# Optimization experiments

Hardware: AMD Instinct MI355X
Metric: run time of the kernel (lower is better)

The kernel has to match this reference:

```python
import jax, jax.numpy as jnp
import numpy as np

N = 100000   # nodes
DEG = 32     # in-degree per node
E = N * DEG  # 3.2M edges
D = 24       # node feature dim
NK = 2       # number of anisotropic kernels (tile(...,2) in source forces 2)
H = 64       # MLP hidden/out channels


def setup_inputs() -> dict:
    key = jax.random.key(0)
    k1, k2, k3, k4 = jax.random.split(key, 4)
    x = jax.random.normal(k1, (N, D), dtype=jnp.float32)
    src = jax.random.randint(k2, (E,), 0, N)
    tgt = jnp.repeat(jnp.arange(N), DEG)  # every node has DEG in-edges -> no 0/0
    edge_index = jnp.stack([src, tgt]).astype(jnp.int64)
    kvals = jax.random.normal(k3, (NK, E), dtype=jnp.float32)
    # Linear(2*D -> H, bias=False), xavier-like scale
    W = jax.random.normal(k4, (H, NK * D), dtype=jnp.float32) * (1.0 / (NK * D))
    return {"x": x, "edge_index": edge_index, "kvals": kvals, "W": W}


def reference(x, edge_index, kvals, W):
    src, tgt = edge_index[0], edge_index[1]
    xs = x[src]  # [E, D] gathered source features
    # per-kernel sparse aggregation: out_k[i] = sum_{e: tgt[e]==i} kvals[k,e] * x[src[e]]
    out = jnp.concatenate(
        [jax.ops.segment_sum(kvals[k][:, None] * xs, tgt, num_segments=N)
         for k in range(NK)], axis=1)  # [N, NK*D]
    # adj_norm: subtract tiled neighbor mean
    deg = jax.ops.segment_sum(jnp.ones((E,), x.dtype), tgt, num_segments=N)  # [N]
    sum_x = jax.ops.segment_sum(xs, tgt, num_segments=N)  # [N, D]
    norm_x = sum_x / deg[:, None]
    out = out - jnp.tile(norm_x, (1, NK)) + jnp.tile(x, (1, NK))
    # MLP: single bias-free linear, no activation
    return out @ W.T  # [N, H]
```

## Files before the change

kernel.cpp:

```cpp
#include <hip/hip_runtime.h>


#define NN   100000
#define DEG  32
#define EE   (NN * DEG)
#define DD   24
#define HH   64
#define NPB  32
#define TPB  256
#define NPW  8
#define PST  56

typedef __attribute__((ext_vector_type(8)))  short short8;
typedef __attribute__((ext_vector_type(16))) float float16;
typedef __attribute__((ext_vector_type(4)))  float f32x4;
typedef __attribute__((ext_vector_type(4)))  int   i32x4;
typedef __attribute__((ext_vector_type(4)))  unsigned short u16x4;

__device__ __forceinline__ unsigned short f2bf(float f) {
    union { float f; unsigned u; } v; v.f = f;
    unsigned r = v.u + 0x7fffu + ((v.u >> 16) & 1u);
    return (unsigned short)(r >> 16);
}

__device__ __forceinline__ float bf2f(unsigned u) {
    union { unsigned i; float f; } v; v.i = u << 16; return v.f;
}

__device__ __forceinline__ unsigned pk(unsigned a, unsigned b) {
    return __builtin_amdgcn_perm(b, a, 0x05040100u);
}

__device__ __forceinline__ short8 mk8(unsigned u0, unsigned u1, unsigned u2, unsigned u3) {
    union { unsigned u[4]; short8 s; } p;
    p.u[0] = u0; p.u[1] = u1; p.u[2] = u2; p.u[3] = u3;
    return p.s;
}

__global__ void xcvt(const float* __restrict__ x, unsigned short* __restrict__ xb, int n4) {
    int i = blockIdx.x * blockDim.x + threadIdx.x;
    if (i < n4) {
        f32x4 v = __builtin_nontemporal_load(((const f32x4*)x) + i);
        u16x4 o;
        o.x = f2bf(v.x); o.y = f2bf(v.y); o.z = f2bf(v.z); o.w = f2bf(v.w);
        __builtin_nontemporal_store(o, ((u16x4*)xb) + i);
    }
}

__global__ __launch_bounds__(TPB, 4) void gnn(
    const unsigned short* __restrict__ xb,
    const int*            __restrict__ ei,
    const float*          __restrict__ kv,
    const float*          __restrict__ W,
    float*                __restrict__ out)
{
    __shared__ int            ei_s[NPB * DEG];
    __shared__ unsigned short kv_s[2 * NPB * DEG];
    __shared__ unsigned short pre_s[NPB * PST];

    const int t    = threadIdx.x;
    const int lane = t & 63;
    const int w    = t >> 6;
    const int m    = lane & 31;
    const int kh   = lane >> 5;
    const int kh8  = kh * 8;
    const int base = blockIdx.x * NPB;
    const int dclamp = (m < DD) ? m : (DD - 1);
    const int m2     = dclamp * 2;
    const char* xbc  = (const char*)xb;

    {
        const size_t eb = (size_t)base * DEG;
        i32x4 ev = __builtin_nontemporal_load(((const i32x4*)(ei + eb)) + t);
        ev.x *= 48; ev.y *= 48; ev.z *= 48; ev.w *= 48;
        ((i32x4*)ei_s)[t] = ev;
        const f32x4 c0 = __builtin_nontemporal_load(((const f32x4*)(kv + eb)) + t);
        const f32x4 c1 = __builtin_nontemporal_load(((const f32x4*)(kv + EE + eb)) + t);
        u16x4 u0, u1;
        u0.x = f2bf(c0.x); u0.y = f2bf(c0.y); u0.z = f2bf(c0.z); u0.w = f2bf(c0.w);
        u1.x = f2bf(c1.x); u1.y = f2bf(c1.y); u1.z = f2bf(c1.z); u1.w = f2bf(c1.w);
        ((u16x4*)kv_s)[t] = u0;
        ((u16x4*)(kv_s + NPB * DEG))[t] = u1;
    }
    __syncthreads();

    const unsigned short* kvrow = kv_s + (m & 1) * (NPB * DEG);

    unsigned g[3][16];
    unsigned xv[3];

    #define LOAD_NODE(nl, sl) do {                                             \
        const int el_ = (nl) * DEG + kh8;                                      \
        const i32x4 s0_ = *(const i32x4*)(ei_s + el_);                         \
        const i32x4 s1_ = *(const i32x4*)(ei_s + el_ + 4);                     \
        const i32x4 s2_ = *(const i32x4*)(ei_s + el_ + 16);                    \
        const i32x4 s3_ = *(const i32x4*)(ei_s + el_ + 20);                    \
        g[sl][0]  = *(const unsigned short*)(xbc + (unsigned)(s0_.x + m2));    \
        g[sl][1]  = *(const unsigned short*)(xbc + (unsigned)(s0_.y + m2));    \
        g[sl][2]  = *(const unsigned short*)(xbc + (unsigned)(s0_.z + m2));    \
        g[sl][3]  = *(const unsigned short*)(xbc + (unsigned)(s0_.w + m2));    \
        g[sl][4]  = *(const unsigned short*)(xbc + (unsigned)(s1_.x + m2));    \
        g[sl][5]  = *(const unsigned short*)(xbc + (unsigned)(s1_.y + m2));    \
        g[sl][6]  = *(const unsigned short*)(xbc + (unsigned)(s1_.z + m2));    \
        g[sl][7]  = *(const unsigned short*)(xbc + (unsigned)(s1_.w + m2));    \
        g[sl][8]  = *(const unsigned short*)(xbc + (unsigned)(s2_.x + m2));    \
        g[sl][9]  = *(const unsigned short*)(xbc + (unsigned)(s2_.y + m2));    \
        g[sl][10] = *(const unsigned short*)(xbc + (unsigned)(s2_.z + m2));    \
        g[sl][11] = *(const unsigned short*)(xbc + (unsigned)(s2_.w + m2));    \
        g[sl][12] = *(const unsigned short*)(xbc + (unsigned)(s3_.x + m2));    \
        g[sl][13] = *(const unsigned short*)(xbc + (unsigned)(s3_.y + m2));    \
        g[sl][14] = *(const unsigned short*)(xbc + (unsigned)(s3_.z + m2));    \
        g[sl][15] = *(const unsigned short*)(xbc + (unsigned)(s3_.w + m2));    \
        xv[sl] = xb[(base + (nl)) * DD + dclamp];                              \
    } while (0)

    LOAD_NODE(w * NPW + 0, 0);
    LOAD_NODE(w * NPW + 1, 1);

    #pragma unroll
    for (int i = 0; i < NPW; ++i) {
        const int cur = i % 3;
        const int nl  = w * NPW + i;
        if (i < NPW - 2) LOAD_NODE(nl + 2, (i + 2) % 3);

        const int el = nl * DEG + kh8;
        const short8 raw0 = *(const short8*)(kvrow + el);
        const short8 raw1 = *(const short8*)(kvrow + el + 16);
        const unsigned fill = (m == 2) ? 0x3F803F80u : 0u;
        const short8 af0 = (m < 2) ? raw0 : mk8(fill, fill, fill, fill);
        const short8 af1 = (m < 2) ? raw1 : mk8(fill, fill, fill, fill);

        const short8 bf0 = mk8(pk(g[cur][0],  g[cur][1]),  pk(g[cur][2],  g[cur][3]),
                               pk(g[cur][4],  g[cur][5]),  pk(g[cur][6],  g[cur][7]));
        const short8 bf1 = mk8(pk(g[cur][8],  g[cur][9]),  pk(g[cur][10], g[cur][11]),
                               pk(g[cur][12], g[cur][13]), pk(g[cur][14], g[cur][15]));

        float16 acc;
        #pragma unroll
        for (int r = 0; r < 16; ++r) acc[r] = 0.f;
        acc = __builtin_amdgcn_mfma_f32_32x32x16_bf16(af0, bf0, acc, 0, 0, 0);
        acc = __builtin_amdgcn_mfma_f32_32x32x16_bf16(af1, bf1, acc, 0, 0, 0);

        if (kh == 0 && m < DD) {
            const float sm = acc[2] * (1.f / 32.f);
            const float pv = bf2f(xv[cur]) - sm;
            pre_s[nl * PST + m]      = f2bf(acc[0] + pv);
            pre_s[nl * PST + 24 + m] = f2bf(acc[1] + pv);
        }
    }
    #undef LOAD_NODE
    __syncthreads();

    if (w < 2) {
        const int h = w * 32 + m;

        float16 acc;
        #pragma unroll
        for (int r = 0; r < 16; ++r) acc[r] = 0.f;

        #pragma unroll
        for (int kc = 0; kc < 3; ++kc) {
            const int c0 = kc * 16 + kh8;
            const short8 af = *(const short8*)(pre_s + m * PST + c0);
            const float* wr = W + h * 48 + c0;
            const f32x4 wA = ((const f32x4*)wr)[0];
            const f32x4 wB = ((const f32x4*)wr)[1];
            const short8 bf = mk8(pk(f2bf(wA.x), f2bf(wA.y)), pk(f2bf(wA.z), f2bf(wA.w)),
                                  pk(f2bf(wB.x), f2bf(wB.y)), pk(f2bf(wB.z), f2bf(wB.w)));
            acc = __builtin_amdgcn_mfma_f32_32x32x16_bf16(af, bf, acc, 0, 0, 0);
        }

        #pragma unroll
        for (int r = 0; r < 16; ++r) {
            const int row = (r & 3) + 8 * (r >> 2) + 4 * kh;
            __builtin_nontemporal_store(acc[r], &out[(size_t)(base + row) * HH + h]);
        }
    }
}

extern "C" void kernel_launch(void* const* d_in, const int* in_sizes, int n_in,
                              void* d_out, int out_size, void* d_ws, size_t ws_size,
                              hipStream_t stream) {
    const float* x  = (const float*)d_in[0];
    const int*   ei = (const int*)d_in[1];
    const float* kv = (const float*)d_in[2];
    const float* W  = (const float*)d_in[3];
    float* out = (float*)d_out;

    unsigned short* xb = (unsigned short*)d_ws;
    const int n4 = NN * DD / 4;
    xcvt<<<(n4 + 255) / 256, 256, 0, stream>>>(x, xb, n4);

    const int grid = NN / NPB;
    gnn<<<grid, TPB, 0, stream>>>(xb, ei, kv, W, out);
}
```

Measured before the change: 131.3 us.

## Gather neighbor rows as 16-byte vectors into swizzled LDS before MFMA

The bf16 copy of x is padded to 32-element (64-byte) rows, so each lane can fetch a 16-byte chunk of a neighbor row instead of issuing many 2-byte scalar gathers. Each wave gathers two nodes' neighbor rows into a per-wave shared-memory staging buffer with an XOR swizzle, then reads the bf16 elements back out to build the MFMA operands, double-buffering the gathers in registers. The aim is fewer, wider global loads. In exchange it uses extra LDS (16 KB per block), which may reduce occupancy, and adds LDS round trips. The padded tail of each row is never written, so those bytes hold whatever was already in the workspace and are read as garbage columns; this looks harmless only because the clamped column index (up to 23) never reaches them.

```diff
diff --git a/kernel.cpp b/kernel.cpp
--- a/kernel.cpp
+++ b/kernel.cpp
@@ -10,6 +10,7 @@
 #define TPB  256
 #define NPW  8
 #define PST  56
+#define XRU  32
 
 typedef __attribute__((ext_vector_type(8)))  short short8;
 typedef __attribute__((ext_vector_type(16))) float float16;
@@ -37,13 +38,15 @@
     return p.s;
 }
 
-__global__ void xcvt(const float* __restrict__ x, unsigned short* __restrict__ xb, int n4) {
-    int i = blockIdx.x * blockDim.x + threadIdx.x;
-    if (i < n4) {
-        f32x4 v = __builtin_nontemporal_load(((const f32x4*)x) + i);
+__global__ void xcvt(const float* __restrict__ x, unsigned short* __restrict__ xb, int n6) {
+    int c = blockIdx.x * blockDim.x + threadIdx.x;
+    if (c < n6) {
+        int row = c / 6;
+        int pos = c - row * 6;
+        f32x4 v = __builtin_nontemporal_load(((const f32x4*)x) + c);
         u16x4 o;
         o.x = f2bf(v.x); o.y = f2bf(v.y); o.z = f2bf(v.z); o.w = f2bf(v.w);
-        __builtin_nontemporal_store(o, ((u16x4*)xb) + i);
+        ((u16x4*)xb)[row * 8 + pos] = o;
     }
 }
 
@@ -57,6 +60,7 @@
     __shared__ int            ei_s[NPB * DEG];
     __shared__ unsigned short kv_s[2 * NPB * DEG];
     __shared__ unsigned short pre_s[NPB * PST];
+    __shared__ unsigned short xs_s[4][64 * XRU];
 
     const int t    = threadIdx.x;
     const int lane = t & 63;
@@ -69,10 +73,16 @@
     const int m2     = dclamp * 2;
     const char* xbc  = (const char*)xb;
 
+    const int er   = lane >> 2;
+    const int q16  = (lane & 3) * 16;
+    char* xsb = (char*)&xs_s[w][0];
+    const unsigned wswz = (unsigned)((lane & 32) << 1);
+    const unsigned fswz = (unsigned)(kh << 6);
+
     {
         const size_t eb = (size_t)base * DEG;
         i32x4 ev = __builtin_nontemporal_load(((const i32x4*)(ei + eb)) + t);
-        ev.x *= 48; ev.y *= 48; ev.z *= 48; ev.w *= 48;
+        ev.x <<= 6; ev.y <<= 6; ev.z <<= 6; ev.w <<= 6;
         ((i32x4*)ei_s)[t] = ev;
         const f32x4 c0 = __builtin_nontemporal_load(((const f32x4*)(kv + eb)) + t);
         const f32x4 c1 = __builtin_nontemporal_load(((const f32x4*)(kv + EE + eb)) + t);
@@ -86,69 +96,76 @@
 
     const unsigned short* kvrow = kv_s + (m & 1) * (NPB * DEG);
 
-    unsigned g[3][16];
-    unsigned xv[3];
-
-    #define LOAD_NODE(nl, sl) do {                                             \
-        const int el_ = (nl) * DEG + kh8;                                      \
-        const i32x4 s0_ = *(const i32x4*)(ei_s + el_);                         \
-        const i32x4 s1_ = *(const i32x4*)(ei_s + el_ + 4);                     \
-        const i32x4 s2_ = *(const i32x4*)(ei_s + el_ + 16);                    \
-        const i32x4 s3_ = *(const i32x4*)(ei_s + el_ + 20);                    \
-        g[sl][0]  = *(const unsigned short*)(xbc + (unsigned)(s0_.x + m2));    \
-        g[sl][1]  = *(const unsigned short*)(xbc + (unsigned)(s0_.y + m2));    \
-        g[sl][2]  = *(const unsigned short*)(xbc + (unsigned)(s0_.z + m2));    \
-        g[sl][3]  = *(const unsigned short*)(xbc + (unsigned)(s0_.w + m2));    \
-        g[sl][4]  = *(const unsigned short*)(xbc + (unsigned)(s1_.x + m2));    \
-        g[sl][5]  = *(const unsigned short*)(xbc + (unsigned)(s1_.y + m2));    \
-        g[sl][6]  = *(const unsigned short*)(xbc + (unsigned)(s1_.z + m2));    \
-        g[sl][7]  = *(const unsigned short*)(xbc + (unsigned)(s1_.w + m2));    \
-        g[sl][8]  = *(const unsigned short*)(xbc + (unsigned)(s2_.x + m2));    \
-        g[sl][9]  = *(const unsigned short*)(xbc + (unsigned)(s2_.y + m2));    \
-        g[sl][10] = *(const unsigned short*)(xbc + (unsigned)(s2_.z + m2));    \
-        g[sl][11] = *(const unsigned short*)(xbc + (unsigned)(s2_.w + m2));    \
-        g[sl][12] = *(const unsigned short*)(xbc + (unsigned)(s3_.x + m2));    \
-        g[sl][13] = *(const unsigned short*)(xbc + (unsigned)(s3_.y + m2));    \
-        g[sl][14] = *(const unsigned short*)(xbc + (unsigned)(s3_.z + m2));    \
-        g[sl][15] = *(const unsigned short*)(xbc + (unsigned)(s3_.w + m2));    \
-        xv[sl] = xb[(base + (nl)) * DD + dclamp];                              \
+    i32x4 G[2][4];
+    unsigned short xvv[2][2];
+
+    #define GATHER_GANG(gg, sl) do {                                           \
+        const int eb_ = (w * NPW + 2 * (gg)) * DEG;                            \
+        const int o0_ = ei_s[eb_ +  0 + er];                                   \
+        const int o1_ = ei_s[eb_ + 16 + er];                                   \
+        const int o2_ = ei_s[eb_ + 32 + er];                                   \
+        const int o3_ = ei_s[eb_ + 48 + er];                                   \
+        G[sl][0] = *(const i32x4*)(xbc + (unsigned)(o0_ + q16));               \
+        G[sl][1] = *(const i32x4*)(xbc + (unsigned)(o1_ + q16));               \
+        G[sl][2] = *(const i32x4*)(xbc + (unsigned)(o2_ + q16));               \
+        G[sl][3] = *(const i32x4*)(xbc + (unsigned)(o3_ + q16));               \
+        xvv[sl][0] = xb[(base + w * NPW + 2 * (gg)) * XRU + dclamp];           \
+        xvv[sl][1] = xb[(base + w * NPW + 2 * (gg) + 1) * XRU + dclamp];       \
     } while (0)
 
-    LOAD_NODE(w * NPW + 0, 0);
-    LOAD_NODE(w * NPW + 1, 1);
+    #define WRITE_GANG(sl) do {                                                \
+        *(i32x4*)(xsb + (((0 * 1024) + er * 64 + q16) ^ wswz)) = G[sl][0];     \
+        *(i32x4*)(xsb + (((1 * 1024) + er * 64 + q16) ^ wswz)) = G[sl][1];     \
+        *(i32x4*)(xsb + (((2 * 1024) + er * 64 + q16) ^ wswz)) = G[sl][2];     \
+        *(i32x4*)(xsb + (((3 * 1024) + er * 64 + q16) ^ wswz)) = G[sl][3];     \
+    } while (0)
+
+    #define COMPUTE_NODE(nn, gg, sl) do {                                      \
+        const int nl_ = w * NPW + 2 * (gg) + (nn);                             \
+        const char* fb_ = xsb + (nn) * 2048 + (kh << 9);                       \
+        unsigned ga_[8], gb_[8];                                               \
+        _Pragma("unroll")                                                      \
+        for (int j = 0; j < 8; ++j)                                            \
+            ga_[j] = *(const unsigned short*)(fb_ + (((j << 6) + m2) ^ fswz)); \
+        _Pragma("unroll")                                                      \
+        for (int j = 0; j < 8; ++j)                                            \
+            gb_[j] = *(const unsigned short*)(fb_ + 1024 + (((j << 6) + m2) ^ fswz)); \
+        const int el_ = nl_ * DEG + kh8;                                       \
+        const short8 raw0_ = *(const short8*)(kvrow + el_);                    \
+        const short8 raw1_ = *(const short8*)(kvrow + el_ + 16);               \
+        const unsigned fill_ = (m == 2) ? 0x3F803F80u : 0u;                    \
+        const short8 af0_ = (m < 2) ? raw0_ : mk8(fill_, fill_, fill_, fill_); \
+        const short8 af1_ = (m < 2) ? raw1_ : mk8(fill_, fill_, fill_, fill_); \
+        const short8 bf0_ = mk8(pk(ga_[0], ga_[1]), pk(ga_[2], ga_[3]),        \
+                                pk(ga_[4], ga_[5]), pk(ga_[6], ga_[7]));       \
+        const short8 bf1_ = mk8(pk(gb_[0], gb_[1]), pk(gb_[2], gb_[3]),        \
+                                pk(gb_[4], gb_[5]), pk(gb_[6], gb_[7]));       \
+        float16 acc_;                                                          \
+        _Pragma("unroll")                                                      \
+        for (int r = 0; r < 16; ++r) acc_[r] = 0.f;                            \
+        acc_ = __builtin_amdgcn_mfma_f32_32x32x16_bf16(af0_, bf0_, acc_, 0, 0, 0); \
+        acc_ = __builtin_amdgcn_mfma_f32_32x32x16_bf16(af1_, bf1_, acc_, 0, 0, 0); \
+        if (kh == 0 && m < DD) {                                               \
+            const float sm_ = acc_[2] * (1.f / 32.f);                          \
+            const float pv_ = bf2f(xvv[sl][nn]) - sm_;                         \
+            pre_s[nl_ * PST + m]      = f2bf(acc_[0] + pv_);                   \
+            pre_s[nl_ * PST + 24 + m] = f2bf(acc_[1] + pv_);                   \
+        }                                                                      \
+    } while (0)
+
+    GATHER_GANG(0, 0);
 
     #pragma unroll
-    for (int i = 0; i < NPW; ++i) {
-        const int cur = i % 3;
-        const int nl  = w * NPW + i;
-        if (i < NPW - 2) LOAD_NODE(nl + 2, (i + 2) % 3);
-
-        const int el = nl * DEG + kh8;
-        const short8 raw0 = *(const short8*)(kvrow + el);
-        const short8 raw1 = *(const short8*)(kvrow + el + 16);
-        const unsigned fill = (m == 2) ? 0x3F803F80u : 0u;
-        const short8 af0 = (m < 2) ? raw0 : mk8(fill, fill, fill, fill);
-        const short8 af1 = (m < 2) ? raw1 : mk8(fill, fill, fill, fill);
-
-        const short8 bf0 = mk8(pk(g[cur][0],  g[cur][1]),  pk(g[cur][2],  g[cur][3]),
-                               pk(g[cur][4],  g[cur][5]),  pk(g[cur][6],  g[cur][7]));
-        const short8 bf1 = mk8(pk(g[cur][8],  g[cur][9]),  pk(g[cur][10], g[cur][11]),
-                               pk(g[cur][12], g[cur][13]), pk(g[cur][14], g[cur][15]));
-
-        float16 acc;
-        #pragma unroll
-        for (int r = 0; r < 16; ++r) acc[r] = 0.f;
-        acc = __builtin_amdgcn_mfma_f32_32x32x16_bf16(af0, bf0, acc, 0, 0, 0);
-        acc = __builtin_amdgcn_mfma_f32_32x32x16_bf16(af1, bf1, acc, 0, 0, 0);
-
-        if (kh == 0 && m < DD) {
-            const float sm = acc[2] * (1.f / 32.f);
-            const float pv = bf2f(xv[cur]) - sm;
-            pre_s[nl * PST + m]      = f2bf(acc[0] + pv);
-            pre_s[nl * PST + 24 + m] = f2bf(acc[1] + pv);
-        }
-    }
-    #undef LOAD_NODE
+    for (int gg = 0; gg < NPW / 2; ++gg) {
+        const int sl = gg & 1;
+        WRITE_GANG(sl);
+        if (gg < NPW / 2 - 1) GATHER_GANG(gg + 1, sl ^ 1);
+        COMPUTE_NODE(0, gg, sl);
+        COMPUTE_NODE(1, gg, sl);
+    }
+    #undef GATHER_GANG
+    #undef WRITE_GANG
+    #undef COMPUTE_NODE
     __syncthreads();
 
     if (w < 2) {
@@ -188,8 +205,8 @@
     float* out = (float*)d_out;
 
     unsigned short* xb = (unsigned short*)d_ws;
-    const int n4 = NN * DD / 4;
-    xcvt<<<(n4 + 255) / 256, 256, 0, stream>>>(x, xb, n4);
+    const int n6 = NN * 6;
+    xcvt<<<(n6 + 255) / 256, 256, 0, stream>>>(x, xb, n6);
 
     const int grid = NN / NPB;
     gnn<<<grid, TPB, 0, stream>>>(xb, ei, kv, W, out);
```

Result: no change. 129.1 us (-1.6%).

## Split feature gather into two passes over 16-dim and 8-dim bf16 slices

Applied to the files above, without the earlier changes.

The bf16 feature table is split into a 16-column slice and an 8-column slice, and the aggregation is split into two kernels, one per slice. Each edge's slice is fetched as a single 32-byte or 16-byte vector load and transposed through swizzled LDS, replacing sixteen scattered 2-byte loads per lane. Each pass has a smaller table footprint, so more of it can stay in cache. In exchange, edge indices and kvals are read and converted twice, an extra launch is added, and intermediate results travel through a global workspace buffer.

```diff
diff --git a/kernel.cpp b/kernel.cpp
--- a/kernel.cpp
+++ b/kernel.cpp
@@ -9,12 +9,12 @@
 #define NPB  32
 #define TPB  256
 #define NPW  8
-#define PST  56
 
 typedef __attribute__((ext_vector_type(8)))  short short8;
 typedef __attribute__((ext_vector_type(16))) float float16;
 typedef __attribute__((ext_vector_type(4)))  float f32x4;
 typedef __attribute__((ext_vector_type(4)))  int   i32x4;
+typedef __attribute__((ext_vector_type(2)))  int   i32x2;
 typedef __attribute__((ext_vector_type(4)))  unsigned short u16x4;
 
 __device__ __forceinline__ unsigned short f2bf(float f) {
@@ -37,26 +37,30 @@
     return p.s;
 }
 
-__global__ void xcvt(const float* __restrict__ x, unsigned short* __restrict__ xb, int n4) {
-    int i = blockIdx.x * blockDim.x + threadIdx.x;
-    if (i < n4) {
-        f32x4 v = __builtin_nontemporal_load(((const f32x4*)x) + i);
+__global__ void xcvt2(const float* __restrict__ x,
+                      unsigned short* __restrict__ xlo,
+                      unsigned short* __restrict__ xhi, int n6) {
+    int c = blockIdx.x * blockDim.x + threadIdx.x;
+    if (c < n6) {
+        const int row = c / 6;
+        const int pos = c - row * 6;
+        f32x4 v = __builtin_nontemporal_load(((const f32x4*)x) + c);
         u16x4 o;
         o.x = f2bf(v.x); o.y = f2bf(v.y); o.z = f2bf(v.z); o.w = f2bf(v.w);
-        __builtin_nontemporal_store(o, ((u16x4*)xb) + i);
-    }
-}
-
-__global__ __launch_bounds__(TPB, 4) void gnn(
-    const unsigned short* __restrict__ xb,
+        if (pos < 4) ((u16x4*)xlo)[row * 4 + pos] = o;
+        else         ((u16x4*)xhi)[row * 2 + (pos - 4)] = o;
+    }
+}
+
+__global__ __launch_bounds__(TPB, 4) void gnnA(
+    const unsigned short* __restrict__ xlo,
     const int*            __restrict__ ei,
     const float*          __restrict__ kv,
-    const float*          __restrict__ W,
-    float*                __restrict__ out)
+    unsigned short*       __restrict__ prew)
 {
     __shared__ int            ei_s[NPB * DEG];
     __shared__ unsigned short kv_s[2 * NPB * DEG];
-    __shared__ unsigned short pre_s[NPB * PST];
+    __shared__ unsigned short xt_s[4][1024];
 
     const int t    = threadIdx.x;
     const int lane = t & 63;
@@ -65,14 +69,16 @@
     const int kh   = lane >> 5;
     const int kh8  = kh * 8;
     const int base = blockIdx.x * NPB;
-    const int dclamp = (m < DD) ? m : (DD - 1);
-    const int m2     = dclamp * 2;
-    const char* xbc  = (const char*)xb;
+    const int dcl  = (m < 16) ? m : 15;
+    const char* xc = (const char*)xlo;
+    const int grow = lane >> 1;
+    const int gh   = (lane & 1) * 16;
+    char* xt = (char*)&xt_s[w][0];
 
     {
         const size_t eb = (size_t)base * DEG;
         i32x4 ev = __builtin_nontemporal_load(((const i32x4*)(ei + eb)) + t);
-        ev.x *= 48; ev.y *= 48; ev.z *= 48; ev.w *= 48;
+        ev.x <<= 5; ev.y <<= 5; ev.z <<= 5; ev.w <<= 5;
         ((i32x4*)ei_s)[t] = ev;
         const f32x4 c0 = __builtin_nontemporal_load(((const f32x4*)(kv + eb)) + t);
         const f32x4 c1 = __builtin_nontemporal_load(((const f32x4*)(kv + EE + eb)) + t);
@@ -86,54 +92,43 @@
 
     const unsigned short* kvrow = kv_s + (m & 1) * (NPB * DEG);
 
-    unsigned g[3][16];
-    unsigned xv[3];
-
-    #define LOAD_NODE(nl, sl) do {                                             \
-        const int el_ = (nl) * DEG + kh8;                                      \
-        const i32x4 s0_ = *(const i32x4*)(ei_s + el_);                         \
-        const i32x4 s1_ = *(const i32x4*)(ei_s + el_ + 4);                     \
-        const i32x4 s2_ = *(const i32x4*)(ei_s + el_ + 16);                    \
-        const i32x4 s3_ = *(const i32x4*)(ei_s + el_ + 20);                    \
-        g[sl][0]  = *(const unsigned short*)(xbc + (unsigned)(s0_.x + m2));    \
-        g[sl][1]  = *(const unsigned short*)(xbc + (unsigned)(s0_.y + m2));    \
-        g[sl][2]  = *(const unsigned short*)(xbc + (unsigned)(s0_.z + m2));    \
-        g[sl][3]  = *(const unsigned short*)(xbc + (unsigned)(s0_.w + m2));    \
-        g[sl][4]  = *(const unsigned short*)(xbc + (unsigned)(s1_.x + m2));    \
-        g[sl][5]  = *(const unsigned short*)(xbc + (unsigned)(s1_.y + m2));    \
-        g[sl][6]  = *(const unsigned short*)(xbc + (unsigned)(s1_.z + m2));    \
-        g[sl][7]  = *(const unsigned short*)(xbc + (unsigned)(s1_.w + m2));    \
-        g[sl][8]  = *(const unsigned short*)(xbc + (unsigned)(s2_.x + m2));    \
-        g[sl][9]  = *(const unsigned short*)(xbc + (unsigned)(s2_.y + m2));    \
-        g[sl][10] = *(const unsigned short*)(xbc + (unsigned)(s2_.z + m2));    \
-        g[sl][11] = *(const unsigned short*)(xbc + (unsigned)(s2_.w + m2));    \
-        g[sl][12] = *(const unsigned short*)(xbc + (unsigned)(s3_.x + m2));    \
-        g[sl][13] = *(const unsigned short*)(xbc + (unsigned)(s3_.y + m2));    \
-        g[sl][14] = *(const unsigned short*)(xbc + (unsigned)(s3_.z + m2));    \
-        g[sl][15] = *(const unsigned short*)(xbc + (unsigned)(s3_.w + m2));    \
-        xv[sl] = xb[(base + (nl)) * DD + dclamp];                              \
-    } while (0)
-
-    LOAD_NODE(w * NPW + 0, 0);
-    LOAD_NODE(w * NPW + 1, 1);
-
-    #pragma unroll
-    for (int i = 0; i < NPW; ++i) {
-        const int cur = i % 3;
-        const int nl  = w * NPW + i;
-        if (i < NPW - 2) LOAD_NODE(nl + 2, (i + 2) % 3);
-
+    i32x4 G[NPW];
+    unsigned xv[NPW];
+
+    #pragma unroll
+    for (int n = 0; n < NPW; ++n)
+        xv[n] = xlo[(size_t)(base + w * NPW + n) * 16 + dcl];
+
+    #pragma unroll
+    for (int n = 0; n < NPW; ++n) {
+        const int off = ei_s[(w * NPW + n) * DEG + grow];
+        G[n] = *(const i32x4*)(xc + (unsigned)(off + gh));
+    }
+
+    #pragma unroll
+    for (int n = 0; n < NPW; ++n) {
+        const int b = (n & 1) * 1024;
+        *(i32x4*)(xt + b + ((grow * 32 + gh) ^ ((grow & 8) << 2))) = G[n];
+
+        unsigned ga[8], gb[8];
+        #pragma unroll
+        for (int j = 0; j < 8; ++j) {
+            const int e0 = kh8 + j, e1 = e0 + 16;
+            ga[j] = *(const unsigned short*)(xt + b + ((e0 * 32 + dcl * 2) ^ ((e0 & 8) << 2)));
+            gb[j] = *(const unsigned short*)(xt + b + ((e1 * 32 + dcl * 2) ^ ((e1 & 8) << 2)));
+        }
+
+        const int nl = w * NPW + n;
         const int el = nl * DEG + kh8;
         const short8 raw0 = *(const short8*)(kvrow + el);
         const short8 raw1 = *(const short8*)(kvrow + el + 16);
         const unsigned fill = (m == 2) ? 0x3F803F80u : 0u;
         const short8 af0 = (m < 2) ? raw0 : mk8(fill, fill, fill, fill);
         const short8 af1 = (m < 2) ? raw1 : mk8(fill, fill, fill, fill);
-
-        const short8 bf0 = mk8(pk(g[cur][0],  g[cur][1]),  pk(g[cur][2],  g[cur][3]),
-                               pk(g[cur][4],  g[cur][5]),  pk(g[cur][6],  g[cur][7]));
-        const short8 bf1 = mk8(pk(g[cur][8],  g[cur][9]),  pk(g[cur][10], g[cur][11]),
-                               pk(g[cur][12], g[cur][13]), pk(g[cur][14], g[cur][15]));
+        const short8 bf0 = mk8(pk(ga[0], ga[1]), pk(ga[2], ga[3]),
+                               pk(ga[4], ga[5]), pk(ga[6], ga[7]));
+        const short8 bf1 = mk8(pk(gb[0], gb[1]), pk(gb[2], gb[3]),
+                               pk(gb[4], gb[5]), pk(gb[6], gb[7]));
 
         float16 acc;
         #pragma unroll
@@ -141,18 +136,124 @@
         acc = __builtin_amdgcn_mfma_f32_32x32x16_bf16(af0, bf0, acc, 0, 0, 0);
         acc = __builtin_amdgcn_mfma_f32_32x32x16_bf16(af1, bf1, acc, 0, 0, 0);
 
-        if (kh == 0 && m < DD) {
+        if (kh == 0 && m < 16) {
             const float sm = acc[2] * (1.f / 32.f);
-            const float pv = bf2f(xv[cur]) - sm;
-            pre_s[nl * PST + m]      = f2bf(acc[0] + pv);
-            pre_s[nl * PST + 24 + m] = f2bf(acc[1] + pv);
-        }
-    }
-    #undef LOAD_NODE
+            const float pv = bf2f(xv[n]) - sm;
+            const size_t pr = (size_t)(base + nl) * 32;
+            __builtin_nontemporal_store(f2bf(acc[0] + pv), &prew[pr + m]);
+            __builtin_nontemporal_store(f2bf(acc[1] + pv), &prew[pr + 16 + m]);
+        }
+    }
+}
+
+__global__ __launch_bounds__(TPB, 4) void gnnB(
+    const unsigned short* __restrict__ xhi,
+    const int*            __restrict__ ei,
+    const float*          __restrict__ kv,
+    const unsigned short* __restrict__ prew,
+    const float*          __restrict__ W,
+    float*                __restrict__ out)
+{
+    __shared__ int            ei_s[NPB * DEG];
+    __shared__ unsigned short kv_s[2 * NPB * DEG];
+    __shared__ unsigned short xt_s[4][768];
+    __shared__ unsigned short pre_s[NPB * 16];
+
+    const int t    = threadIdx.x;
+    const int lane = t & 63;
+    const int w    = t >> 6;
+    const int m    = lane & 31;
+    const int kh   = lane >> 5;
+    const int kh8  = kh * 8;
+    const int base = blockIdx.x * NPB;
+    const int dcl  = (m < 8) ? m : 7;
+    const char* xc = (const char*)xhi;
+    const int grow = lane >> 1;
+    const int gh   = (lane & 1) * 8;
+    char* xt = (char*)&xt_s[w][0];
+
+    {
+        const size_t eb = (size_t)base * DEG;
+        i32x4 ev = __builtin_nontemporal_load(((const i32x4*)(ei + eb)) + t);
+        ev.x <<= 4; ev.y <<= 4; ev.z <<= 4; ev.w <<= 4;
+        ((i32x4*)ei_s)[t] = ev;
+        const f32x4 c0 = __builtin_nontemporal_load(((const f32x4*)(kv + eb)) + t);
+        const f32x4 c1 = __builtin_nontemporal_load(((const f32x4*)(kv + EE + eb)) + t);
+        u16x4 u0, u1;
+        u0.x = f2bf(c0.x); u0.y = f2bf(c0.y); u0.z = f2bf(c0.z); u0.w = f2bf(c0.w);
+        u1.x = f2bf(c1.x); u1.y = f2bf(c1.y); u1.z = f2bf(c1.z); u1.w = f2bf(c1.w);
+        ((u16x4*)kv_s)[t] = u0;
+        ((u16x4*)(kv_s + NPB * DEG))[t] = u1;
+    }
+    __syncthreads();
+
+    const unsigned short* kvrow = kv_s + (m & 1) * (NPB * DEG);
+
+    i32x4 wsA, wsB, wsC;
+    if (w < 2) {
+        const unsigned short* pr = prew + (size_t)(base + m) * 32;
+        wsA = *(const i32x4*)(pr + kh8);
+        wsB = *(const i32x4*)(pr + 16);
+        wsC = *(const i32x4*)(pr + 24);
+    }
+
+    i32x2 G[NPW];
+    unsigned xv[NPW];
+
+    #pragma unroll
+    for (int n = 0; n < NPW; ++n)
+        xv[n] = xhi[(size_t)(base + w * NPW + n) * 8 + dcl];
+
+    #pragma unroll
+    for (int n = 0; n < NPW; ++n) {
+        const int off = ei_s[(w * NPW + n) * DEG + grow];
+        G[n] = *(const i32x2*)(xc + (unsigned)(off + gh));
+    }
+
+    #pragma unroll
+    for (int n = 0; n < NPW; ++n) {
+        const int b = (n & 1) * 768;
+        *(i32x2*)(xt + b + grow * 24 + gh) = G[n];
+
+        unsigned ga[8], gb[8];
+        #pragma unroll
+        for (int j = 0; j < 8; ++j) {
+            const int e0 = kh8 + j, e1 = e0 + 16;
+            ga[j] = *(const unsigned short*)(xt + b + e0 * 24 + dcl * 2);
+            gb[j] = *(const unsigned short*)(xt + b + e1 * 24 + dcl * 2);
+        }
+
+        const int nl = w * NPW + n;
+        const int el = nl * DEG + kh8;
+        const short8 raw0 = *(const short8*)(kvrow + el);
+        const short8 raw1 = *(const short8*)(kvrow + el + 16);
+        const unsigned fill = (m == 2) ? 0x3F803F80u : 0u;
+        const short8 af0 = (m < 2) ? raw0 : mk8(fill, fill, fill, fill);
+        const short8 af1 = (m < 2) ? raw1 : mk8(fill, fill, fill, fill);
+        const short8 bf0 = mk8(pk(ga[0], ga[1]), pk(ga[2], ga[3]),
+                               pk(ga[4], ga[5]), pk(ga[6], ga[7]));
+        const short8 bf1 = mk8(pk(gb[0], gb[1]), pk(gb[2], gb[3]),
+                               pk(gb[4], gb[5]), pk(gb[6], gb[7]));
+
+        float16 acc;
+        #pragma unroll
+        for (int r = 0; r < 16; ++r) acc[r] = 0.f;
+        acc = __builtin_amdgcn_mfma_f32_32x32x16_bf16(af0, bf0, acc, 0, 0, 0);
+        acc = __builtin_amdgcn_mfma_f32_32x32x16_bf16(af1, bf1, acc, 0, 0, 0);
+
+        if (kh == 0 && m < 8) {
+            const float sm = acc[2] * (1.f / 32.f);
+            const float pv = bf2f(xv[n]) - sm;
+            pre_s[nl * 16 + m]     = f2bf(acc[0] + pv);
+            pre_s[nl * 16 + 8 + m] = f2bf(acc[1] + pv);
+        }
+    }
     __syncthreads();
 
     if (w < 2) {
         const int h = w * 32 + m;
+        union { i32x4 v; short8 s; } uA, uB, uC;
+        uA.v = wsA; uB.v = wsB; uC.v = wsC;
 
         float16 acc;
         #pragma unroll
@@ -160,9 +261,17 @@
 
         #pragma unroll
         for (int kc = 0; kc < 3; ++kc) {
-            const int c0 = kc * 16 + kh8;
-            const short8 af = *(const short8*)(pre_s + m * PST + c0);
-            const float* wr = W + h * 48 + c0;
+            short8 af;
+            if (kc == 0) {
+                af = uA.s;
+            } else if (kc == 1) {
+                const short8 l = *(const short8*)(pre_s + m * 16);
+                af = (kh == 0) ? l : uB.s;
+            } else {
+                const short8 l = *(const short8*)(pre_s + m * 16 + 8);
+                af = (kh == 0) ? uC.s : l;
+            }
+            const float* wr = W + h * 48 + kc * 16 + kh8;
             const f32x4 wA = ((const f32x4*)wr)[0];
             const f32x4 wB = ((const f32x4*)wr)[1];
             const short8 bf = mk8(pk(f2bf(wA.x), f2bf(wA.y)), pk(f2bf(wA.z), f2bf(wA.w)),
@@ -187,10 +296,14 @@
     const float* W  = (const float*)d_in[3];
     float* out = (float*)d_out;
 
-    unsigned short* xb = (unsigned short*)d_ws;
-    const int n4 = NN * DD / 4;
-    xcvt<<<(n4 + 255) / 256, 256, 0, stream>>>(x, xb, n4);
+    unsigned short* xlo  = (unsigned short*)d_ws;
+    unsigned short* xhi  = xlo + (size_t)NN * 16;
+    unsigned short* prew = xhi + (size_t)NN * 8;
+
+    const int n6 = NN * 6;
+    xcvt2<<<(n6 + 255) / 256, 256, 0, stream>>>(x, xlo, xhi, n6);
 
     const int grid = NN / NPB;
-    gnn<<<grid, TPB, 0, stream>>>(xb, ei, kv, W, out);
-}
+    gnnA<<<grid, TPB, 0, stream>>>(xlo, ei, kv, prew);
+    gnnB<<<grid, TPB, 0, stream>>>(xhi, ei, kv, prew, W, out);
+}
```

Result: slower. 149.5 us (+13.9%).
